# Performance work log

Hardware: AMD Instinct MI355X
Metric: run time of the kernel (lower is better)

The kernel has to match this reference:

```python
import jax, jax.numpy as jnp
import numpy as np

B, S, D, H = 2, 4096, 768, 12
DH = D // H
SCALE = 1.0 / DH ** 0.5


def setup_inputs() -> dict:
    key = jax.random.key(0)
    k1, k2, k3, k4, k5 = jax.random.split(key, 5)
    x = jax.random.normal(k1, (B, S, D), dtype=jnp.float32)
    # nn.Linear weights: stored as [out, in]; init ~ U(-1/sqrt(in), 1/sqrt(in))
    lim = 1.0 / np.sqrt(D)
    W_qkv = jax.random.uniform(k2, (3 * D, D), minval=-lim, maxval=lim, dtype=jnp.float32)
    b_qkv = jax.random.uniform(k3, (3 * D,), minval=-lim, maxval=lim, dtype=jnp.float32)
    W_out = jax.random.uniform(k4, (D, D), minval=-lim, maxval=lim, dtype=jnp.float32)
    b_out = jax.random.uniform(k5, (D,), minval=-lim, maxval=lim, dtype=jnp.float32)
    return {"x": x, "W_qkv": W_qkv, "b_qkv": b_qkv, "W_out": W_out, "b_out": b_out}


def reference(x, W_qkv, b_qkv, W_out, b_out):
    bs, ns, _ = x.shape
    qkv = x @ W_qkv.T + b_qkv                       # [B, S, 3D]
    qkv = qkv.reshape(bs, ns, 3, H, DH)
    qkv = jnp.transpose(qkv, (2, 0, 3, 1, 4))        # [3, B, H, S, DH]
    q, k, v = qkv[0], qkv[1], qkv[2]
    attn = jnp.einsum('bhqd,bhkd->bhqk', q, k)       # [B, H, S, S]
    attn = jax.nn.softmax(attn * SCALE, axis=-1)
    out = jnp.einsum('bhqk,bhkd->bhqd', attn, v)     # [B, H, S, DH]
    out = jnp.transpose(out, (0, 2, 1, 3)).reshape(bs, ns, D)
    return out @ W_out.T + b_out
```

## Files before the change

### kernel.cpp

```cpp
#include <hip/hip_runtime.h>
#include <hip/hip_bf16.h>
#include <stdint.h>

#define B_    2
#define S_    4096
#define D_    768
#define H_    12
#define DH_   64
#define BH_   (B_*H_)
#define M_    (B_*S_)
#define NQKV_ 2304
#define QSCALE_ 0.18033688011112042f

typedef unsigned short bf16u;
typedef short bf16x8 __attribute__((ext_vector_type(8)));
typedef float f32x4 __attribute__((ext_vector_type(4)));

__device__ __forceinline__ bf16u f2bf(float f) {
    unsigned u = __float_as_uint(f);
    u += 0x7FFFu + ((u >> 16) & 1u);
    return (bf16u)(u >> 16);
}

__device__ __forceinline__ void gl_lds16(const void* g, void* l) {
    __builtin_amdgcn_global_load_lds(
        (const __attribute__((address_space(1))) unsigned*)g,
        (__attribute__((address_space(3))) unsigned*)l, 16, 0, 0);
}

__global__ __launch_bounds__(256) void convert_kernel(
    const float* __restrict__ src, bf16u* __restrict__ dst, int n4)
{
    int i = blockIdx.x * 256 + threadIdx.x;
    if (i < n4) {
        float4 v = ((const float4*)src)[i];
        ushort4 o;
        o.x = f2bf(v.x); o.y = f2bf(v.y); o.z = f2bf(v.z); o.w = f2bf(v.w);
        ((ushort4*)dst)[i] = o;
    }
}

template<int EPI>
__global__ __launch_bounds__(256) void gemm_kernel(
    const bf16u* __restrict__ A, const bf16u* __restrict__ Bw,
    const float* __restrict__ bias, float* __restrict__ Cout,
    bf16u* __restrict__ Qb, bf16u* __restrict__ Kb, bf16u* __restrict__ Vtb)
{
    __shared__ bf16u As[128*32];
    __shared__ bf16u Bs[128*32];
    const int tid  = threadIdx.x;
    const int lane = tid & 63;
    const int wave = tid >> 6;
    const int wr = wave >> 1, wc = wave & 1;
    const int lr = lane & 15;
    const int quad = lane >> 4;
    const int m0 = blockIdx.y * 128;
    const int n0 = blockIdx.x * 128;

    f32x4 acc[4][4];
    #pragma unroll
    for (int i = 0; i < 4; i++)
        #pragma unroll
        for (int j = 0; j < 4; j++)
            acc[i][j] = (f32x4){0.f, 0.f, 0.f, 0.f};

    for (int k0 = 0; k0 < 768; k0 += 32) {
        #pragma unroll
        for (int r = 0; r < 2; r++) {
            int c = r * 256 + tid;
            int row = c >> 2;
            int col = ((c & 3) ^ (row & 3)) * 8;
            gl_lds16(A  + (size_t)(m0 + row) * 768 + k0 + col, (char*)As + c * 16);
            gl_lds16(Bw + (size_t)(n0 + row) * 768 + k0 + col, (char*)Bs + c * 16);
        }
        __syncthreads();
        bf16x8 af[4], bg[4];
        #pragma unroll
        for (int t = 0; t < 4; t++) {
            int ra = wr * 64 + t * 16 + lr;
            int rb = wc * 64 + t * 16 + lr;
            af[t] = *(const bf16x8*)(As + ra * 32 + ((quad ^ (ra & 3)) * 8));
            bg[t] = *(const bf16x8*)(Bs + rb * 32 + ((quad ^ (rb & 3)) * 8));
        }
        #pragma unroll
        for (int i = 0; i < 4; i++)
            #pragma unroll
            for (int j = 0; j < 4; j++)
                acc[i][j] = __builtin_amdgcn_mfma_f32_16x16x32_bf16(
                    af[i], bg[j], acc[i][j], 0, 0, 0);
        __syncthreads();
    }

    #pragma unroll
    for (int i = 0; i < 4; i++) {
        int mbase = m0 + wr * 64 + i * 16 + quad * 4;
        #pragma unroll
        for (int j = 0; j < 4; j++) {
            int n = n0 + wc * 64 + j * 16 + lr;
            float bv = bias[n];
            if (EPI == 0) {
                #pragma unroll
                for (int r = 0; r < 4; r++)
                    Cout[(size_t)(mbase + r) * 768 + n] = acc[i][j][r] + bv;
            } else {
                int t3  = n / 768;
                int rem = n - t3 * 768;
                int h   = rem >> 6;
                int dh  = rem & 63;
                #pragma unroll
                for (int r = 0; r < 4; r++) {
                    int mm = mbase + r;
                    int b  = mm >> 12;
                    int s  = mm & 4095;
                    int bh = b * H_ + h;
                    float v = acc[i][j][r] + bv;
                    if (t3 == 0)
                        Qb[((size_t)bh * S_ + s) * DH_ + dh] = f2bf(v * QSCALE_);
                    else if (t3 == 1)
                        Kb[((size_t)bh * S_ + s) * DH_ + dh] = f2bf(v);
                    else
                        Vtb[((size_t)bh * DH_ + dh) * S_ + s] = f2bf(v);
                }
            }
        }
    }
}

#define PS_STRIDE 72

__global__ __launch_bounds__(256, 3) void attn_kernel(
    const bf16u* __restrict__ Qb, const bf16u* __restrict__ Kb,
    const bf16u* __restrict__ Vtb, bf16u* __restrict__ A2)
{
    __shared__ bf16u Ks[2][64*64];
    __shared__ bf16u Vs[2][64*64];
    __shared__ bf16u Ps[4][32*PS_STRIDE];
    const int tid  = threadIdx.x;
    const int lane = tid & 63;
    const int w    = tid >> 6;
    const int lr   = lane & 15;
    const int quad = lane >> 4;
    const int q0   = blockIdx.x * 128;
    const int bh   = blockIdx.y;

    const size_t kbase_g = (size_t)bh * S_ * DH_;
    const size_t vbase_g = (size_t)bh * DH_ * S_;

    bf16x8 aq[2][2];
    #pragma unroll
    for (int rh = 0; rh < 2; rh++) {
        const size_t qb = ((size_t)bh * S_ + q0 + w * 32 + rh * 16 + lr) * DH_ + quad * 8;
        aq[rh][0] = *(const bf16x8*)(Qb + qb);
        aq[rh][1] = *(const bf16x8*)(Qb + qb + 32);
    }

    bf16x8 onesf;
    #pragma unroll
    for (int j = 0; j < 8; j++) onesf[j] = (short)0x3F80;

    f32x4 o[2][4];
    f32x4 l_acc[2];
    #pragma unroll
    for (int rh = 0; rh < 2; rh++) {
        l_acc[rh] = (f32x4){0.f, 0.f, 0.f, 0.f};
        #pragma unroll
        for (int t = 0; t < 4; t++)
            o[rh][t] = (f32x4){0.f, 0.f, 0.f, 0.f};
    }

    int kvoff[4][2];
    #pragma unroll
    for (int nt = 0; nt < 4; nt++) {
        int rk = nt * 16 + lr;
        kvoff[nt][0] = rk * 64 + ((quad ^ (rk & 7)) * 8);
        kvoff[nt][1] = rk * 64 + (((4 + quad) ^ (rk & 7)) * 8);
    }
    bf16u* pw[2];
    #pragma unroll
    for (int rh = 0; rh < 2; rh++)
        pw[rh] = &Ps[w][(rh * 16 + lr) * PS_STRIDE];

    auto stage = [&](int kv0, int bf) {
        #pragma unroll
        for (int r = 0; r < 2; r++) {
            int c = r * 256 + tid;
            int row = c >> 3;
            int col = ((c & 7) ^ (row & 7)) * 8;
            gl_lds16(Kb  + kbase_g + (size_t)(kv0 + row) * DH_ + col,
                     (char*)&Ks[bf][0] + c * 16);
            gl_lds16(Vtb + vbase_g + (size_t)row * S_ + kv0 + col,
                     (char*)&Vs[bf][0] + c * 16);
        }
    };

    stage(0, 0);

    auto body = [&](int it, int buf, bool do_stage) __attribute__((always_inline)) {
        __syncthreads();
        if (do_stage) stage((it + 1) * 64, buf ^ 1);

        const bf16u* Kbuf = &Ks[buf][0];
        const bf16u* Vbuf = &Vs[buf][0];

        f32x4 sc[2][4];
        __builtin_amdgcn_s_setprio(1);
        #pragma unroll
        for (int nt = 0; nt < 4; nt++) {
            const bf16x8 bk0 = *(const bf16x8*)(Kbuf + kvoff[nt][0]);
            const bf16x8 bk1 = *(const bf16x8*)(Kbuf + kvoff[nt][1]);
            #pragma unroll
            for (int rh = 0; rh < 2; rh++) {
                f32x4 s = (f32x4){0.f, 0.f, 0.f, 0.f};
                s = __builtin_amdgcn_mfma_f32_16x16x32_bf16(bk0, aq[rh][0], s, 0, 0, 0);
                s = __builtin_amdgcn_mfma_f32_16x16x32_bf16(bk1, aq[rh][1], s, 0, 0, 0);
                sc[rh][nt] = s;
            }
        }
        __builtin_amdgcn_s_setprio(0);

        #pragma unroll
        for (int rh = 0; rh < 2; rh++) {
            #pragma unroll
            for (int nt = 0; nt < 4; nt++) {
                float p0 = __builtin_amdgcn_exp2f(sc[rh][nt][0]);
                float p1 = __builtin_amdgcn_exp2f(sc[rh][nt][1]);
                float p2 = __builtin_amdgcn_exp2f(sc[rh][nt][2]);
                float p3 = __builtin_amdgcn_exp2f(sc[rh][nt][3]);
                unsigned w0 = __builtin_amdgcn_perm(__float_as_uint(p1),
                                                    __float_as_uint(p0), 0x07060302u);
                unsigned w1 = __builtin_amdgcn_perm(__float_as_uint(p3),
                                                    __float_as_uint(p2), 0x07060302u);
                *(uint2*)(pw[rh] + nt * 16 + quad * 4) = make_uint2(w0, w1);
            }
        }

        __asm__ volatile("s_waitcnt lgkmcnt(0)" ::: "memory");

        __builtin_amdgcn_s_setprio(1);
        #pragma unroll
        for (int rh = 0; rh < 2; rh++) {
            const bf16x8 ap0 = *(const bf16x8*)(pw[rh] + quad * 8);
            const bf16x8 ap1 = *(const bf16x8*)(pw[rh] + 32 + quad * 8);
            l_acc[rh] = __builtin_amdgcn_mfma_f32_16x16x32_bf16(ap0, onesf, l_acc[rh], 0, 0, 0);
            l_acc[rh] = __builtin_amdgcn_mfma_f32_16x16x32_bf16(ap1, onesf, l_acc[rh], 0, 0, 0);
            #pragma unroll
            for (int nt = 0; nt < 4; nt++) {
                const bf16x8 bv0 = *(const bf16x8*)(Vbuf + kvoff[nt][0]);
                const bf16x8 bv1 = *(const bf16x8*)(Vbuf + kvoff[nt][1]);
                o[rh][nt] = __builtin_amdgcn_mfma_f32_16x16x32_bf16(ap0, bv0, o[rh][nt], 0, 0, 0);
                o[rh][nt] = __builtin_amdgcn_mfma_f32_16x16x32_bf16(ap1, bv1, o[rh][nt], 0, 0, 0);
            }
        }
        __builtin_amdgcn_s_setprio(0);
    };

    #pragma unroll 1
    for (int it = 0; it < S_ / 64 - 2; it += 2) {
        body(it,     0, true);
        body(it + 1, 1, true);
    }
    body(S_ / 64 - 2, 0, true);
    body(S_ / 64 - 1, 1, false);

    const int b = bh / H_, h = bh % H_;
    #pragma unroll
    for (int rh = 0; rh < 2; rh++) {
        float rl[4];
        #pragma unroll
        for (int r2 = 0; r2 < 4; r2++) rl[r2] = 1.0f / l_acc[rh][r2];
        #pragma unroll
        for (int nt = 0; nt < 4; nt++)
            #pragma unroll
            for (int r2 = 0; r2 < 4; r2++) {
                int q = q0 + w * 32 + rh * 16 + quad * 4 + r2;
                float v = o[rh][nt][r2] * rl[r2];
                A2[((size_t)b * S_ + q) * D_ + h * DH_ + nt * 16 + lr] = f2bf(v);
            }
    }
}

extern "C" void kernel_launch(void* const* d_in, const int* in_sizes, int n_in,
                              void* d_out, int out_size, void* d_ws, size_t ws_size,
                              hipStream_t stream) {
    const float* x     = (const float*)d_in[0];
    const float* W_qkv = (const float*)d_in[1];
    const float* b_qkv = (const float*)d_in[2];
    const float* W_out = (const float*)d_in[3];
    const float* b_out = (const float*)d_in[4];
    float* out = (float*)d_out;
    char* ws = (char*)d_ws;

    bf16u* xb    = (bf16u*)(ws + 0);
    bf16u* wqkvb = (bf16u*)(ws + 12582912);
    bf16u* woutb = (bf16u*)(ws + 16121856);
    bf16u* Qb    = (bf16u*)(ws + 17301504);
    bf16u* Kb    = (bf16u*)(ws + 29884416);
    bf16u* Vtb   = (bf16u*)(ws + 42467328);
    bf16u* A2    = (bf16u*)(ws + 55050240);

    convert_kernel<<<6291456/4/256, 256, 0, stream>>>(x, xb, 6291456/4);
    convert_kernel<<<1769472/4/256, 256, 0, stream>>>(W_qkv, wqkvb, 1769472/4);
    convert_kernel<<< 589824/4/256, 256, 0, stream>>>(W_out, woutb, 589824/4);

    dim3 g1(NQKV_/128, M_/128);
    gemm_kernel<1><<<g1, 256, 0, stream>>>(xb, wqkvb, b_qkv, nullptr, Qb, Kb, Vtb);

    dim3 g2(S_/128, BH_);
    attn_kernel<<<g2, 256, 0, stream>>>(Qb, Kb, Vtb, A2);

    dim3 g3(D_/128, M_/128);
    gemm_kernel<0><<<g3, 256, 0, stream>>>(A2, woutb, b_out, out, nullptr, nullptr, nullptr);
}
```

Baseline: 282.8 us.

## Restructure attention to 8 waves with register-level P transpose and XCD-aware block remap

The attention kernel now runs 8 waves of 16 query rows each instead of 4 waves of 32. The P matrix is moved from the score layout to the MFMA A-operand layout with permlane32/permlane16 swaps rather than a round trip through LDS, which removes the Ps buffer and its lgkmcnt wait. Both the attention and GEMM kernels remap block indices so that consecutive blocks sharing K/V or operands land on the same XCD for L2 reuse. The cost is that each K/V tile is now consumed by more waves with fewer MFMAs per LDS read, and the swizzle relies on exact grid shapes.

```diff
diff --git a/kernel.cpp b/kernel.cpp
--- a/kernel.cpp
+++ b/kernel.cpp
@@ -54,8 +54,12 @@
     const int wr = wave >> 1, wc = wave & 1;
     const int lr = lane & 15;
     const int quad = lane >> 4;
-    const int m0 = blockIdx.y * 128;
-    const int n0 = blockIdx.x * 128;
+
+    const int nwg  = gridDim.x * gridDim.y;
+    const int fblk = blockIdx.y * gridDim.x + blockIdx.x;
+    const int vblk = (fblk & 7) * (nwg >> 3) + (fblk >> 3);
+    const int m0 = (vblk / gridDim.x) * 128;
+    const int n0 = (vblk % gridDim.x) * 128;
 
     f32x4 acc[4][4];
     #pragma unroll
@@ -126,71 +130,57 @@
     }
 }
 
-#define PS_STRIDE 72
-
-__global__ __launch_bounds__(256, 3) void attn_kernel(
+__global__ __launch_bounds__(512, 6) void attn_kernel(
     const bf16u* __restrict__ Qb, const bf16u* __restrict__ Kb,
     const bf16u* __restrict__ Vtb, bf16u* __restrict__ A2)
 {
-    __shared__ bf16u Ks[2][64*64];
-    __shared__ bf16u Vs[2][64*64];
-    __shared__ bf16u Ps[4][32*PS_STRIDE];
+    __shared__ char Lds[32768];
     const int tid  = threadIdx.x;
     const int lane = tid & 63;
     const int w    = tid >> 6;
     const int lr   = lane & 15;
     const int quad = lane >> 4;
-    const int q0   = blockIdx.x * 128;
-    const int bh   = blockIdx.y;
+
+    const int fblk = blockIdx.y * gridDim.x + blockIdx.x;
+    const int vblk = (fblk & 7) * 96 + (fblk >> 3);
+    const int q0   = (vblk & 31) * 128;
+    const int bh   = vblk >> 5;
 
     const size_t kbase_g = (size_t)bh * S_ * DH_;
     const size_t vbase_g = (size_t)bh * DH_ * S_;
 
-    bf16x8 aq[2][2];
-    #pragma unroll
-    for (int rh = 0; rh < 2; rh++) {
-        const size_t qb = ((size_t)bh * S_ + q0 + w * 32 + rh * 16 + lr) * DH_ + quad * 8;
-        aq[rh][0] = *(const bf16x8*)(Qb + qb);
-        aq[rh][1] = *(const bf16x8*)(Qb + qb + 32);
+    bf16x8 aq0, aq1;
+    {
+        const size_t qb = ((size_t)bh * S_ + q0 + w * 16 + lr) * DH_ + quad * 8;
+        aq0 = *(const bf16x8*)(Qb + qb);
+        aq1 = *(const bf16x8*)(Qb + qb + 32);
     }
 
     bf16x8 onesf;
     #pragma unroll
     for (int j = 0; j < 8; j++) onesf[j] = (short)0x3F80;
 
-    f32x4 o[2][4];
-    f32x4 l_acc[2];
-    #pragma unroll
-    for (int rh = 0; rh < 2; rh++) {
-        l_acc[rh] = (f32x4){0.f, 0.f, 0.f, 0.f};
-        #pragma unroll
-        for (int t = 0; t < 4; t++)
-            o[rh][t] = (f32x4){0.f, 0.f, 0.f, 0.f};
-    }
-
-    int kvoff[4][2];
+    f32x4 o[4];
+    f32x4 l_acc = (f32x4){0.f, 0.f, 0.f, 0.f};
+    #pragma unroll
+    for (int t = 0; t < 4; t++) o[t] = (f32x4){0.f, 0.f, 0.f, 0.f};
+
+    int kvaddr[4][2];
     #pragma unroll
     for (int nt = 0; nt < 4; nt++) {
         int rk = nt * 16 + lr;
-        kvoff[nt][0] = rk * 64 + ((quad ^ (rk & 7)) * 8);
-        kvoff[nt][1] = rk * 64 + (((4 + quad) ^ (rk & 7)) * 8);
-    }
-    bf16u* pw[2];
-    #pragma unroll
-    for (int rh = 0; rh < 2; rh++)
-        pw[rh] = &Ps[w][(rh * 16 + lr) * PS_STRIDE];
+        kvaddr[nt][0] = (rk * 64 + ((quad ^ (rk & 7)) * 8)) * 2;
+        kvaddr[nt][1] = (rk * 64 + (((4 + quad) ^ (rk & 7)) * 8)) * 2;
+    }
 
     auto stage = [&](int kv0, int bf) {
-        #pragma unroll
-        for (int r = 0; r < 2; r++) {
-            int c = r * 256 + tid;
-            int row = c >> 3;
-            int col = ((c & 7) ^ (row & 7)) * 8;
-            gl_lds16(Kb  + kbase_g + (size_t)(kv0 + row) * DH_ + col,
-                     (char*)&Ks[bf][0] + c * 16);
-            gl_lds16(Vtb + vbase_g + (size_t)row * S_ + kv0 + col,
-                     (char*)&Vs[bf][0] + c * 16);
-        }
+        int c = tid;
+        int row = c >> 3;
+        int col = ((c & 7) ^ (row & 7)) * 8;
+        gl_lds16(Kb  + kbase_g + (size_t)(kv0 + row) * DH_ + col,
+                 Lds + bf * 8192 + c * 16);
+        gl_lds16(Vtb + vbase_g + (size_t)row * S_ + kv0 + col,
+                 Lds + 16384 + bf * 8192 + c * 16);
     };
 
     stage(0, 0);
@@ -199,57 +189,60 @@
         __syncthreads();
         if (do_stage) stage((it + 1) * 64, buf ^ 1);
 
-        const bf16u* Kbuf = &Ks[buf][0];
-        const bf16u* Vbuf = &Vs[buf][0];
-
-        f32x4 sc[2][4];
+        const char* Kbuf = Lds + buf * 8192;
+        const char* Vbuf = Lds + 16384 + buf * 8192;
+
+        f32x4 sc[4];
         __builtin_amdgcn_s_setprio(1);
         #pragma unroll
         for (int nt = 0; nt < 4; nt++) {
-            const bf16x8 bk0 = *(const bf16x8*)(Kbuf + kvoff[nt][0]);
-            const bf16x8 bk1 = *(const bf16x8*)(Kbuf + kvoff[nt][1]);
+            const bf16x8 bk0 = *(const bf16x8*)(Kbuf + kvaddr[nt][0]);
+            const bf16x8 bk1 = *(const bf16x8*)(Kbuf + kvaddr[nt][1]);
+            f32x4 s = (f32x4){0.f, 0.f, 0.f, 0.f};
+            s = __builtin_amdgcn_mfma_f32_16x16x32_bf16(bk0, aq0, s, 0, 0, 0);
+            s = __builtin_amdgcn_mfma_f32_16x16x32_bf16(bk1, aq1, s, 0, 0, 0);
+            sc[nt] = s;
+        }
+        __builtin_amdgcn_s_setprio(0);
+
+        unsigned W[4][2];
+        #pragma unroll
+        for (int nt = 0; nt < 4; nt++) {
+            float p0 = __builtin_amdgcn_exp2f(sc[nt][0]);
+            float p1 = __builtin_amdgcn_exp2f(sc[nt][1]);
+            float p2 = __builtin_amdgcn_exp2f(sc[nt][2]);
+            float p3 = __builtin_amdgcn_exp2f(sc[nt][3]);
+            W[nt][0] = __builtin_amdgcn_perm(__float_as_uint(p1),
+                                             __float_as_uint(p0), 0x07060302u);
+            W[nt][1] = __builtin_amdgcn_perm(__float_as_uint(p3),
+                                             __float_as_uint(p2), 0x07060302u);
+        }
+
+        bf16x8 ap[2];
+        #pragma unroll
+        for (int ks = 0; ks < 2; ks++) {
+            union { unsigned u[4]; bf16x8 v; } Af;
             #pragma unroll
-            for (int rh = 0; rh < 2; rh++) {
-                f32x4 s = (f32x4){0.f, 0.f, 0.f, 0.f};
-                s = __builtin_amdgcn_mfma_f32_16x16x32_bf16(bk0, aq[rh][0], s, 0, 0, 0);
-                s = __builtin_amdgcn_mfma_f32_16x16x32_bf16(bk1, aq[rh][1], s, 0, 0, 0);
-                sc[rh][nt] = s;
+            for (int b = 0; b < 2; b++) {
+                auto r1 = __builtin_amdgcn_permlane32_swap(
+                    W[2 * ks][b], W[2 * ks + 1][b], false, false);
+                auto r2 = __builtin_amdgcn_permlane16_swap(
+                    r1[0], r1[1], false, false);
+                Af.u[b]     = r2[0];
+                Af.u[2 + b] = r2[1];
             }
-        }
-        __builtin_amdgcn_s_setprio(0);
-
-        #pragma unroll
-        for (int rh = 0; rh < 2; rh++) {
-            #pragma unroll
-            for (int nt = 0; nt < 4; nt++) {
-                float p0 = __builtin_amdgcn_exp2f(sc[rh][nt][0]);
-                float p1 = __builtin_amdgcn_exp2f(sc[rh][nt][1]);
-                float p2 = __builtin_amdgcn_exp2f(sc[rh][nt][2]);
-                float p3 = __builtin_amdgcn_exp2f(sc[rh][nt][3]);
-                unsigned w0 = __builtin_amdgcn_perm(__float_as_uint(p1),
-                                                    __float_as_uint(p0), 0x07060302u);
-                unsigned w1 = __builtin_amdgcn_perm(__float_as_uint(p3),
-                                                    __float_as_uint(p2), 0x07060302u);
-                *(uint2*)(pw[rh] + nt * 16 + quad * 4) = make_uint2(w0, w1);
-            }
-        }
-
-        __asm__ volatile("s_waitcnt lgkmcnt(0)" ::: "memory");
+            ap[ks] = Af.v;
+        }
 
         __builtin_amdgcn_s_setprio(1);
-        #pragma unroll
-        for (int rh = 0; rh < 2; rh++) {
-            const bf16x8 ap0 = *(const bf16x8*)(pw[rh] + quad * 8);
-            const bf16x8 ap1 = *(const bf16x8*)(pw[rh] + 32 + quad * 8);
-            l_acc[rh] = __builtin_amdgcn_mfma_f32_16x16x32_bf16(ap0, onesf, l_acc[rh], 0, 0, 0);
-            l_acc[rh] = __builtin_amdgcn_mfma_f32_16x16x32_bf16(ap1, onesf, l_acc[rh], 0, 0, 0);
-            #pragma unroll
-            for (int nt = 0; nt < 4; nt++) {
-                const bf16x8 bv0 = *(const bf16x8*)(Vbuf + kvoff[nt][0]);
-                const bf16x8 bv1 = *(const bf16x8*)(Vbuf + kvoff[nt][1]);
-                o[rh][nt] = __builtin_amdgcn_mfma_f32_16x16x32_bf16(ap0, bv0, o[rh][nt], 0, 0, 0);
-                o[rh][nt] = __builtin_amdgcn_mfma_f32_16x16x32_bf16(ap1, bv1, o[rh][nt], 0, 0, 0);
-            }
+        l_acc = __builtin_amdgcn_mfma_f32_16x16x32_bf16(ap[0], onesf, l_acc, 0, 0, 0);
+        l_acc = __builtin_amdgcn_mfma_f32_16x16x32_bf16(ap[1], onesf, l_acc, 0, 0, 0);
+        #pragma unroll
+        for (int nt = 0; nt < 4; nt++) {
+            const bf16x8 bv0 = *(const bf16x8*)(Vbuf + kvaddr[nt][0]);
+            const bf16x8 bv1 = *(const bf16x8*)(Vbuf + kvaddr[nt][1]);
+            o[nt] = __builtin_amdgcn_mfma_f32_16x16x32_bf16(ap[0], bv0, o[nt], 0, 0, 0);
+            o[nt] = __builtin_amdgcn_mfma_f32_16x16x32_bf16(ap[1], bv1, o[nt], 0, 0, 0);
         }
         __builtin_amdgcn_s_setprio(0);
     };
@@ -263,20 +256,17 @@
     body(S_ / 64 - 1, 1, false);
 
     const int b = bh / H_, h = bh % H_;
-    #pragma unroll
-    for (int rh = 0; rh < 2; rh++) {
-        float rl[4];
-        #pragma unroll
-        for (int r2 = 0; r2 < 4; r2++) rl[r2] = 1.0f / l_acc[rh][r2];
-        #pragma unroll
-        for (int nt = 0; nt < 4; nt++)
-            #pragma unroll
-            for (int r2 = 0; r2 < 4; r2++) {
-                int q = q0 + w * 32 + rh * 16 + quad * 4 + r2;
-                float v = o[rh][nt][r2] * rl[r2];
-                A2[((size_t)b * S_ + q) * D_ + h * DH_ + nt * 16 + lr] = f2bf(v);
-            }
-    }
+    float rl[4];
+    #pragma unroll
+    for (int r2 = 0; r2 < 4; r2++) rl[r2] = 1.0f / l_acc[r2];
+    #pragma unroll
+    for (int nt = 0; nt < 4; nt++)
+        #pragma unroll
+        for (int r2 = 0; r2 < 4; r2++) {
+            int q = q0 + w * 16 + quad * 4 + r2;
+            float v = o[nt][r2] * rl[r2];
+            A2[((size_t)b * S_ + q) * D_ + h * DH_ + nt * 16 + lr] = f2bf(v);
+        }
 }
 
 extern "C" void kernel_launch(void* const* d_in, const int* in_sizes, int n_in,
@@ -306,7 +296,7 @@
     gemm_kernel<1><<<g1, 256, 0, stream>>>(xb, wqkvb, b_qkv, nullptr, Qb, Kb, Vtb);
 
     dim3 g2(S_/128, BH_);
-    attn_kernel<<<g2, 256, 0, stream>>>(Qb, Kb, Vtb, A2);
+    attn_kernel<<<g2, 512, 0, stream>>>(Qb, Kb, Vtb, A2);
 
     dim3 g3(D_/128, M_/128);
     gemm_kernel<0><<<g3, 256, 0, stream>>>(A2, woutb, b_out, out, nullptr, nullptr, nullptr);
```

Measured after the change: 273.2 us. -3.4%, faster.
